# Kernel tuning notes

Measured on AMD Instinct MI355X. Metric: run time of the kernel, lower is better.

The kernel has to match this reference:

```python
import jax, jax.numpy as jnp
import numpy as np

HIDDEN = 32
N_STEPS = 64  # fixed-step RK4 replaces adaptive Dopri5 (same MLP-eval structure)
STD = 0.1     # init_params: Linear weights ~ N(0, 0.1), biases = 0


def _mlp(w1, b1, w2, b2, w3, b3, y):
    # NODE.forward: fc1 -> relu -> fc2 -> relu -> fc3 (t is unused in the source)
    h = jax.nn.relu(y @ w1 + b1)
    h = jax.nn.relu(h @ w2 + b2)
    return h @ w3 + b3


def setup_inputs() -> dict:
    key = jax.random.key(0)
    ks = jax.random.split(key, 8)
    B, D = 131072, 3
    x = jax.random.normal(ks[0], (B, D), dtype=jnp.float32)
    # eval times in (0.1, 1.0], sorted like a posterior-sample schedule
    samples = jnp.sort(
        jax.random.uniform(ks[1], (8, 1), jnp.float32, 0.1, 1.0), axis=0)
    w1 = (STD * jax.random.normal(ks[2], (D, HIDDEN))).astype(jnp.float32)
    b1 = jnp.zeros((HIDDEN,), jnp.float32)
    w2 = (STD * jax.random.normal(ks[3], (HIDDEN, HIDDEN))).astype(jnp.float32)
    b2 = jnp.zeros((HIDDEN,), jnp.float32)
    w3 = (STD * jax.random.normal(ks[4], (HIDDEN, D))).astype(jnp.float32)
    b3 = jnp.zeros((D,), jnp.float32)
    w_out = (STD * jax.random.normal(ks[5], (D, 1))).astype(jnp.float32)
    b_out = jnp.zeros((1,), jnp.float32)
    return {"x": x, "samples": samples, "w1": w1, "b1": b1, "w2": w2,
            "b2": b2, "w3": w3, "b3": b3, "w_out": w_out, "b_out": b_out}


def reference(x, samples, w1, b1, w2, b2, w3, b3, w_out, b_out):
    t_eval = samples[:, 0]                     # (S,)
    max_T = jnp.max(t_eval)
    dt = max_T / N_STEPS

    def step(y, _):
        k1 = _mlp(w1, b1, w2, b2, w3, b3, y)
        k2 = _mlp(w1, b1, w2, b2, w3, b3, y + 0.5 * dt * k1)
        k3 = _mlp(w1, b1, w2, b2, w3, b3, y + 0.5 * dt * k2)
        k4 = _mlp(w1, b1, w2, b2, w3, b3, y + dt * k3)
        y_new = y + (dt / 6.0) * (k1 + 2.0 * k2 + 2.0 * k3 + k4)
        return y_new, y_new

    # traj[i] is the state at time (i+1)*dt; shape (N_STEPS, B, 3)
    _, traj = jax.lax.scan(jax.checkpoint(step), x, jnp.arange(N_STEPS))

    # gather states at the grid step nearest each eval time
    idx = jnp.clip(jnp.round(t_eval / dt).astype(jnp.int32) - 1, 0, N_STEPS - 1)
    y_eval = traj[idx]                         # (S, B, 3)

    # fc_layers readout -> act_vec (S, B, 1)
    return y_eval @ w_out + b_out
```

## Files before the change

### kernel.cpp

```cpp
#include <hip/hip_runtime.h>

#define NSTEPS 64

typedef __attribute__((ext_vector_type(4)))  float  float4_;
typedef __attribute__((ext_vector_type(2)))  __fp16 half2_;
typedef __attribute__((ext_vector_type(8)))  __fp16 half8_;

__device__ __forceinline__ half2_ relu_pk_f16(float a, float b) {
    half2_ h = __builtin_amdgcn_cvt_pkrtz(a, b);
    return __builtin_elementwise_max(h, (half2_)(__fp16)0);
}

__global__ __launch_bounds__(64, 4)
void ode_rk4_mfma(const float* __restrict__ x,
                  const float* __restrict__ samples,
                  const float* __restrict__ w1, const float* __restrict__ b1,
                  const float* __restrict__ w2, const float* __restrict__ b2,
                  const float* __restrict__ w3, const float* __restrict__ b3,
                  const float* __restrict__ w_out, const float* __restrict__ b_out,
                  float* __restrict__ out, int B)
{
    const int lane  = threadIdx.x & 63;
    const int col16 = lane & 15;
    const int quad  = lane >> 4;

    const int row = blockIdx.x * 16 + col16;

    auto sig = [](int p) -> int {
        int q = (p & 15) >> 2, r = p & 3;
        return q * 8 + r + ((p < 16) ? 0 : 4);
    };

    const float maxT = samples[7];
    const float dt   = maxT / 64.0f;
    const float dt2  = 0.5f * dt;
    const float dt6  = dt / 6.0f;

    union F { half2_ h2[4]; half8_ h8; };

    F Mh[2], Mz[2];
#pragma unroll
    for (int H = 0; H < 2; ++H) {
        int u = sig(16 * H + col16);
#pragma unroll
        for (int pp = 0; pp < 4; ++pp) {
            int kk = quad * 8 + 2 * pp;
            float m0 = w3[kk * 3 + 0] * w1[0 * 32 + u]
                     + w3[kk * 3 + 1] * w1[1 * 32 + u]
                     + w3[kk * 3 + 2] * w1[2 * 32 + u];
            float m1 = w3[(kk + 1) * 3 + 0] * w1[0 * 32 + u]
                     + w3[(kk + 1) * 3 + 1] * w1[1 * 32 + u]
                     + w3[(kk + 1) * 3 + 2] * w1[2 * 32 + u];
            Mh[H].h2[pp] = (half2_){(__fp16)(dt2 * m0), (__fp16)(dt2 * m1)};
            Mz[H].h2[pp] = (half2_){(__fp16)(dt6 * m0), (__fp16)(dt6 * m1)};
        }
    }

    F A2[2];
    float4_ Cb[2];
#pragma unroll
    for (int H = 0; H < 2; ++H) {
        int u = sig(16 * H + col16);
#pragma unroll
        for (int pp = 0; pp < 4; ++pp) {
            int kk = quad * 8 + 2 * pp;
            A2[H].h2[pp] = (half2_){(__fp16)w2[kk * 32 + u], (__fp16)w2[(kk + 1) * 32 + u]};
        }
#pragma unroll
        for (int r = 0; r < 4; ++r)
            Cb[H][r] = b2[sig(16 * H + quad * 4 + r)];
    }

    F A3;
    {
        const int  d    = col16 & 3;
        const bool live = d < 3;
#pragma unroll
        for (int pp = 0; pp < 4; ++pp) {
            int kk = quad * 8 + 2 * pp;
            A3.h2[pp] = live
                ? (half2_){(__fp16)w3[kk * 3 + d], (__fp16)w3[(kk + 1) * 3 + d]}
                : (half2_)(__fp16)0.0f;
        }
    }
    float4_ C3;
#pragma unroll
    for (int r = 0; r < 4; ++r)
        C3[r] = (r < 3) ? 6.0f * b3[r] : 0.0f;

    float4_ cH[2];
#pragma unroll
    for (int H = 0; H < 2; ++H)
#pragma unroll
        for (int r = 0; r < 4; ++r) {
            int u = sig(16 * H + quad * 4 + r);
            cH[H][r] = dt2 * (b3[0] * w1[0 * 32 + u] + b3[1] * w1[1 * 32 + u] + b3[2] * w1[2 * 32 + u]);
        }

    int sidx[8];
    unsigned long long smask = 0ull;
#pragma unroll
    for (int j = 0; j < 8; ++j) {
        int id = (int)rintf(samples[j] / dt) - 1;
        id = id < 0 ? 0 : (id > NSTEPS - 1 ? NSTEPS - 1 : id);
        id = __builtin_amdgcn_readfirstlane(id);
        sidx[j] = id;
        smask |= 1ull << id;
    }
    const float wo0 = w_out[0], wo1 = w_out[1], wo2 = w_out[2];
    const float bo  = b_out[0];

    float y0 = x[(size_t)row * 3 + 0];
    float y1 = x[(size_t)row * 3 + 1];
    float y2 = x[(size_t)row * 3 + 2];

    float4_ zb0, zb1;
    {
        F A1y[2];
#pragma unroll
        for (int H = 0; H < 2; ++H) {
            if (quad == 0) {
                int u = sig(16 * H + col16);
                A1y[H].h2[0] = (half2_){(__fp16)w1[0 * 32 + u], (__fp16)w1[1 * 32 + u]};
                A1y[H].h2[1] = (half2_){(__fp16)w1[2 * 32 + u], (__fp16)b1[u]};
                A1y[H].h2[2] = (half2_)(__fp16)0.0f;
                A1y[H].h2[3] = (half2_)(__fp16)0.0f;
            } else {
#pragma unroll
                for (int pp = 0; pp < 4; ++pp) A1y[H].h2[pp] = (half2_)(__fp16)0.0f;
            }
        }
        float4_ Zc;
#pragma unroll
        for (int r = 0; r < 4; ++r) Zc[r] = 0.0f;
        half2_ b0a = __builtin_amdgcn_cvt_pkrtz(y0, y1);
        half2_ b0b = __builtin_amdgcn_cvt_pkrtz(y2, 1.0f);
        F By;
        By.h2[0] = b0a; By.h2[1] = b0b; By.h2[2] = b0a; By.h2[3] = b0b;
        zb0 = __builtin_amdgcn_mfma_f32_16x16x32_f16(A1y[0].h8, By.h8, Zc, 0, 0, 0);
        zb1 = __builtin_amdgcn_mfma_f32_16x16x32_f16(A1y[1].h8, By.h8, Zc, 0, 0, 0);
    }

    const half2_ two = (half2_)(__fp16)2.0f;

#pragma unroll 1
    for (int s = 0; s < NSTEPS; ++s) {
        F P, Q, S;

        P.h2[0] = relu_pk_f16(zb0[0], zb0[1]);
        P.h2[1] = relu_pk_f16(zb0[2], zb0[3]);
        P.h2[2] = relu_pk_f16(zb1[0], zb1[1]);
        P.h2[3] = relu_pk_f16(zb1[2], zb1[3]);
        __builtin_amdgcn_s_setprio(1);
        float4_ D2_0 = __builtin_amdgcn_mfma_f32_16x16x32_f16(A2[0].h8, P.h8, Cb[0], 0, 0, 0);
        float4_ D2_1 = __builtin_amdgcn_mfma_f32_16x16x32_f16(A2[1].h8, P.h8, Cb[1], 0, 0, 0);
        __builtin_amdgcn_s_setprio(0);
        Q.h2[0] = relu_pk_f16(D2_0[0], D2_0[1]);
        Q.h2[1] = relu_pk_f16(D2_0[2], D2_0[3]);
        Q.h2[2] = relu_pk_f16(D2_1[0], D2_1[1]);
        Q.h2[3] = relu_pk_f16(D2_1[2], D2_1[3]);
#pragma unroll
        for (int pp = 0; pp < 4; ++pp) S.h2[pp] = Q.h2[pp];

        float4_ zh0 = zb0 + cH[0];
        float4_ zh1 = zb1 + cH[1];

#pragma unroll
        for (int st = 1; st <= 2; ++st) {
            __builtin_amdgcn_s_setprio(1);
            float4_ D1_0 = __builtin_amdgcn_mfma_f32_16x16x32_f16(Mh[0].h8, Q.h8, zh0, 0, 0, 0);
            float4_ D1_1 = __builtin_amdgcn_mfma_f32_16x16x32_f16(Mh[1].h8, Q.h8, zh1, 0, 0, 0);
            __builtin_amdgcn_s_setprio(0);
            P.h2[0] = relu_pk_f16(D1_0[0], D1_0[1]);
            P.h2[1] = relu_pk_f16(D1_0[2], D1_0[3]);
            P.h2[2] = relu_pk_f16(D1_1[0], D1_1[1]);
            P.h2[3] = relu_pk_f16(D1_1[2], D1_1[3]);
            __builtin_amdgcn_s_setprio(1);
            float4_ E0 = __builtin_amdgcn_mfma_f32_16x16x32_f16(A2[0].h8, P.h8, Cb[0], 0, 0, 0);
            float4_ E1 = __builtin_amdgcn_mfma_f32_16x16x32_f16(A2[1].h8, P.h8, Cb[1], 0, 0, 0);
            __builtin_amdgcn_s_setprio(0);
            Q.h2[0] = relu_pk_f16(E0[0], E0[1]);
            Q.h2[1] = relu_pk_f16(E0[2], E0[3]);
            Q.h2[2] = relu_pk_f16(E1[0], E1[1]);
            Q.h2[3] = relu_pk_f16(E1[2], E1[3]);
#pragma unroll
            for (int pp = 0; pp < 4; ++pp)
                S.h2[pp] += two * Q.h2[pp];
        }

        zh0 = zh0 + cH[0];
        zh1 = zh1 + cH[1];
        F Qd;
#pragma unroll
        for (int pp = 0; pp < 4; ++pp) Qd.h2[pp] = Q.h2[pp] + Q.h2[pp];
        __builtin_amdgcn_s_setprio(1);
        float4_ D1_0 = __builtin_amdgcn_mfma_f32_16x16x32_f16(Mh[0].h8, Qd.h8, zh0, 0, 0, 0);
        float4_ D1_1 = __builtin_amdgcn_mfma_f32_16x16x32_f16(Mh[1].h8, Qd.h8, zh1, 0, 0, 0);
        __builtin_amdgcn_s_setprio(0);
        P.h2[0] = relu_pk_f16(D1_0[0], D1_0[1]);
        P.h2[1] = relu_pk_f16(D1_0[2], D1_0[3]);
        P.h2[2] = relu_pk_f16(D1_1[0], D1_1[1]);
        P.h2[3] = relu_pk_f16(D1_1[2], D1_1[3]);
        __builtin_amdgcn_s_setprio(1);
        float4_ E0 = __builtin_amdgcn_mfma_f32_16x16x32_f16(A2[0].h8, P.h8, Cb[0], 0, 0, 0);
        float4_ E1 = __builtin_amdgcn_mfma_f32_16x16x32_f16(A2[1].h8, P.h8, Cb[1], 0, 0, 0);
        __builtin_amdgcn_s_setprio(0);
        Q.h2[0] = relu_pk_f16(E0[0], E0[1]);
        Q.h2[1] = relu_pk_f16(E0[2], E0[3]);
        Q.h2[2] = relu_pk_f16(E1[0], E1[1]);
        Q.h2[3] = relu_pk_f16(E1[2], E1[3]);
#pragma unroll
        for (int pp = 0; pp < 4; ++pp) S.h2[pp] += Q.h2[pp];

        __builtin_amdgcn_s_setprio(1);
        float4_ D3 = __builtin_amdgcn_mfma_f32_16x16x32_f16(A3.h8, S.h8, C3, 0, 0, 0);
        zb0 = __builtin_amdgcn_mfma_f32_16x16x32_f16(Mz[0].h8, S.h8, zb0, 0, 0, 0);
        zb1 = __builtin_amdgcn_mfma_f32_16x16x32_f16(Mz[1].h8, S.h8, zb1, 0, 0, 0);
        __builtin_amdgcn_s_setprio(0);
#pragma unroll
        for (int r = 0; r < 4; ++r) {
            zb0[r] = fmaf(2.0f, cH[0][r], zb0[r]);
            zb1[r] = fmaf(2.0f, cH[1][r], zb1[r]);
        }
        y0 = fmaf(dt6, D3[0], y0);
        y1 = fmaf(dt6, D3[1], y1);
        y2 = fmaf(dt6, D3[2], y2);

        if ((smask >> s) & 1ull) {
            if (quad == 0) {
#pragma unroll
                for (int j = 0; j < 8; ++j) {
                    if (sidx[j] == s) {
                        out[(size_t)j * B + row] = fmaf(y2, wo2, fmaf(y1, wo1, fmaf(y0, wo0, bo)));
                    }
                }
            }
        }
    }
}

extern "C" void kernel_launch(void* const* d_in, const int* in_sizes, int n_in,
                              void* d_out, int out_size, void* d_ws, size_t ws_size,
                              hipStream_t stream) {
    const float* x       = (const float*)d_in[0];
    const float* samples = (const float*)d_in[1];
    const float* w1      = (const float*)d_in[2];
    const float* b1      = (const float*)d_in[3];
    const float* w2      = (const float*)d_in[4];
    const float* b2      = (const float*)d_in[5];
    const float* w3      = (const float*)d_in[6];
    const float* b3      = (const float*)d_in[7];
    const float* w_out   = (const float*)d_in[8];
    const float* b_out   = (const float*)d_in[9];
    float* out = (float*)d_out;

    const int B = in_sizes[0] / 3;
    const int rowsPerBlock = 16;
    const int grid = (B + rowsPerBlock - 1) / rowsPerBlock;
    ode_rk4_mfma<<<grid, 64, 0, stream>>>(
        x, samples, w1, b1, w2, b2, w3, b3, w_out, b_out, out, B);
}
```

Baseline: 208.9 us.

## Process two independent 16-row tiles per wavefront to interleave MFMA chains

Each wavefront now integrates two 16-row batches, running the RK4 step for both inside the same loop iteration. Because the two steps share no data, the compiler can interleave their dependent MFMA/ReLU chains and hide MFMA latency without relying on other waves. The s_setprio hints are removed, the grid is halved, and launch bounds drop to 3 waves per EU to make room for the doubled register state. The risk is lower occupancy and possible register pressure if the compiler serializes the two chains.

```diff
diff --git a/kernel.cpp b/kernel.cpp
--- a/kernel.cpp
+++ b/kernel.cpp
@@ -11,7 +11,7 @@
     return __builtin_elementwise_max(h, (half2_)(__fp16)0);
 }
 
-__global__ __launch_bounds__(64, 4)
+__global__ __launch_bounds__(64, 3)
 void ode_rk4_mfma(const float* __restrict__ x,
                   const float* __restrict__ samples,
                   const float* __restrict__ w1, const float* __restrict__ b1,
@@ -24,7 +24,8 @@
     const int col16 = lane & 15;
     const int quad  = lane >> 4;
 
-    const int row = blockIdx.x * 16 + col16;
+    const int rowA = blockIdx.x * 32 + col16;
+    const int rowB = rowA + 16;
 
     auto sig = [](int p) -> int {
         int q = (p & 15) >> 2, r = p & 3;
@@ -110,11 +111,14 @@
     const float wo0 = w_out[0], wo1 = w_out[1], wo2 = w_out[2];
     const float bo  = b_out[0];
 
-    float y0 = x[(size_t)row * 3 + 0];
-    float y1 = x[(size_t)row * 3 + 1];
-    float y2 = x[(size_t)row * 3 + 2];
-
-    float4_ zb0, zb1;
+    float yA0 = x[(size_t)rowA * 3 + 0];
+    float yA1 = x[(size_t)rowA * 3 + 1];
+    float yA2 = x[(size_t)rowA * 3 + 2];
+    float yB0 = x[(size_t)rowB * 3 + 0];
+    float yB1 = x[(size_t)rowB * 3 + 1];
+    float yB2 = x[(size_t)rowB * 3 + 2];
+
+    float4_ zbA0, zbA1, zbB0, zbB1;
     {
         F A1y[2];
 #pragma unroll
@@ -133,28 +137,29 @@
         float4_ Zc;
 #pragma unroll
         for (int r = 0; r < 4; ++r) Zc[r] = 0.0f;
-        half2_ b0a = __builtin_amdgcn_cvt_pkrtz(y0, y1);
-        half2_ b0b = __builtin_amdgcn_cvt_pkrtz(y2, 1.0f);
-        F By;
-        By.h2[0] = b0a; By.h2[1] = b0b; By.h2[2] = b0a; By.h2[3] = b0b;
-        zb0 = __builtin_amdgcn_mfma_f32_16x16x32_f16(A1y[0].h8, By.h8, Zc, 0, 0, 0);
-        zb1 = __builtin_amdgcn_mfma_f32_16x16x32_f16(A1y[1].h8, By.h8, Zc, 0, 0, 0);
+        half2_ aA = __builtin_amdgcn_cvt_pkrtz(yA0, yA1);
+        half2_ bA = __builtin_amdgcn_cvt_pkrtz(yA2, 1.0f);
+        half2_ aB = __builtin_amdgcn_cvt_pkrtz(yB0, yB1);
+        half2_ bB = __builtin_amdgcn_cvt_pkrtz(yB2, 1.0f);
+        F ByA, ByB;
+        ByA.h2[0] = aA; ByA.h2[1] = bA; ByA.h2[2] = aA; ByA.h2[3] = bA;
+        ByB.h2[0] = aB; ByB.h2[1] = bB; ByB.h2[2] = aB; ByB.h2[3] = bB;
+        zbA0 = __builtin_amdgcn_mfma_f32_16x16x32_f16(A1y[0].h8, ByA.h8, Zc, 0, 0, 0);
+        zbA1 = __builtin_amdgcn_mfma_f32_16x16x32_f16(A1y[1].h8, ByA.h8, Zc, 0, 0, 0);
+        zbB0 = __builtin_amdgcn_mfma_f32_16x16x32_f16(A1y[0].h8, ByB.h8, Zc, 0, 0, 0);
+        zbB1 = __builtin_amdgcn_mfma_f32_16x16x32_f16(A1y[1].h8, ByB.h8, Zc, 0, 0, 0);
     }
 
     const half2_ two = (half2_)(__fp16)2.0f;
 
-#pragma unroll 1
-    for (int s = 0; s < NSTEPS; ++s) {
+    auto rk_step = [&](float4_& zb0, float4_& zb1, float& y0, float& y1, float& y2) {
         F P, Q, S;
-
         P.h2[0] = relu_pk_f16(zb0[0], zb0[1]);
         P.h2[1] = relu_pk_f16(zb0[2], zb0[3]);
         P.h2[2] = relu_pk_f16(zb1[0], zb1[1]);
         P.h2[3] = relu_pk_f16(zb1[2], zb1[3]);
-        __builtin_amdgcn_s_setprio(1);
         float4_ D2_0 = __builtin_amdgcn_mfma_f32_16x16x32_f16(A2[0].h8, P.h8, Cb[0], 0, 0, 0);
         float4_ D2_1 = __builtin_amdgcn_mfma_f32_16x16x32_f16(A2[1].h8, P.h8, Cb[1], 0, 0, 0);
-        __builtin_amdgcn_s_setprio(0);
         Q.h2[0] = relu_pk_f16(D2_0[0], D2_0[1]);
         Q.h2[1] = relu_pk_f16(D2_0[2], D2_0[3]);
         Q.h2[2] = relu_pk_f16(D2_1[0], D2_1[1]);
@@ -167,18 +172,14 @@
 
 #pragma unroll
         for (int st = 1; st <= 2; ++st) {
-            __builtin_amdgcn_s_setprio(1);
             float4_ D1_0 = __builtin_amdgcn_mfma_f32_16x16x32_f16(Mh[0].h8, Q.h8, zh0, 0, 0, 0);
             float4_ D1_1 = __builtin_amdgcn_mfma_f32_16x16x32_f16(Mh[1].h8, Q.h8, zh1, 0, 0, 0);
-            __builtin_amdgcn_s_setprio(0);
             P.h2[0] = relu_pk_f16(D1_0[0], D1_0[1]);
             P.h2[1] = relu_pk_f16(D1_0[2], D1_0[3]);
             P.h2[2] = relu_pk_f16(D1_1[0], D1_1[1]);
             P.h2[3] = relu_pk_f16(D1_1[2], D1_1[3]);
-            __builtin_amdgcn_s_setprio(1);
             float4_ E0 = __builtin_amdgcn_mfma_f32_16x16x32_f16(A2[0].h8, P.h8, Cb[0], 0, 0, 0);
             float4_ E1 = __builtin_amdgcn_mfma_f32_16x16x32_f16(A2[1].h8, P.h8, Cb[1], 0, 0, 0);
-            __builtin_amdgcn_s_setprio(0);
             Q.h2[0] = relu_pk_f16(E0[0], E0[1]);
             Q.h2[1] = relu_pk_f16(E0[2], E0[3]);
             Q.h2[2] = relu_pk_f16(E1[0], E1[1]);
@@ -193,18 +194,14 @@
         F Qd;
 #pragma unroll
         for (int pp = 0; pp < 4; ++pp) Qd.h2[pp] = Q.h2[pp] + Q.h2[pp];
-        __builtin_amdgcn_s_setprio(1);
         float4_ D1_0 = __builtin_amdgcn_mfma_f32_16x16x32_f16(Mh[0].h8, Qd.h8, zh0, 0, 0, 0);
         float4_ D1_1 = __builtin_amdgcn_mfma_f32_16x16x32_f16(Mh[1].h8, Qd.h8, zh1, 0, 0, 0);
-        __builtin_amdgcn_s_setprio(0);
         P.h2[0] = relu_pk_f16(D1_0[0], D1_0[1]);
         P.h2[1] = relu_pk_f16(D1_0[2], D1_0[3]);
         P.h2[2] = relu_pk_f16(D1_1[0], D1_1[1]);
         P.h2[3] = relu_pk_f16(D1_1[2], D1_1[3]);
-        __builtin_amdgcn_s_setprio(1);
         float4_ E0 = __builtin_amdgcn_mfma_f32_16x16x32_f16(A2[0].h8, P.h8, Cb[0], 0, 0, 0);
         float4_ E1 = __builtin_amdgcn_mfma_f32_16x16x32_f16(A2[1].h8, P.h8, Cb[1], 0, 0, 0);
-        __builtin_amdgcn_s_setprio(0);
         Q.h2[0] = relu_pk_f16(E0[0], E0[1]);
         Q.h2[1] = relu_pk_f16(E0[2], E0[3]);
         Q.h2[2] = relu_pk_f16(E1[0], E1[1]);
@@ -212,11 +209,9 @@
 #pragma unroll
         for (int pp = 0; pp < 4; ++pp) S.h2[pp] += Q.h2[pp];
 
-        __builtin_amdgcn_s_setprio(1);
         float4_ D3 = __builtin_amdgcn_mfma_f32_16x16x32_f16(A3.h8, S.h8, C3, 0, 0, 0);
         zb0 = __builtin_amdgcn_mfma_f32_16x16x32_f16(Mz[0].h8, S.h8, zb0, 0, 0, 0);
         zb1 = __builtin_amdgcn_mfma_f32_16x16x32_f16(Mz[1].h8, S.h8, zb1, 0, 0, 0);
-        __builtin_amdgcn_s_setprio(0);
 #pragma unroll
         for (int r = 0; r < 4; ++r) {
             zb0[r] = fmaf(2.0f, cH[0][r], zb0[r]);
@@ -225,13 +220,20 @@
         y0 = fmaf(dt6, D3[0], y0);
         y1 = fmaf(dt6, D3[1], y1);
         y2 = fmaf(dt6, D3[2], y2);
+    };
+
+#pragma unroll 1
+    for (int s = 0; s < NSTEPS; ++s) {
+        rk_step(zbA0, zbA1, yA0, yA1, yA2);
+        rk_step(zbB0, zbB1, yB0, yB1, yB2);
 
         if ((smask >> s) & 1ull) {
             if (quad == 0) {
 #pragma unroll
                 for (int j = 0; j < 8; ++j) {
                     if (sidx[j] == s) {
-                        out[(size_t)j * B + row] = fmaf(y2, wo2, fmaf(y1, wo1, fmaf(y0, wo0, bo)));
+                        out[(size_t)j * B + rowA] = fmaf(yA2, wo2, fmaf(yA1, wo1, fmaf(yA0, wo0, bo)));
+                        out[(size_t)j * B + rowB] = fmaf(yB2, wo2, fmaf(yB1, wo1, fmaf(yB0, wo0, bo)));
                     }
                 }
             }
@@ -255,7 +257,7 @@
     float* out = (float*)d_out;
 
     const int B = in_sizes[0] / 3;
-    const int rowsPerBlock = 16;
+    const int rowsPerBlock = 32;
     const int grid = (B + rowsPerBlock - 1) / rowsPerBlock;
     ode_rk4_mfma<<<grid, 64, 0, stream>>>(
         x, samples, w1, b1, w2, b2, w3, b3, w_out, b_out, out, B);
```

Result: slower. 214.2 us (+2.5%).

## Accumulate stage sums in fp16 and defer the y readout to sample steps

Applied to the files above, without the earlier changes.

The per-step y update through the w3 MFMA is removed. A running fp16 sum of stage activations is kept instead, and y is rebuilt only at sample steps with one MFMA plus a linear bias term. The 2*Q doubling before the last stage is replaced by a separate Mf matrix scaled by dt, and the setprio hints are dropped. The launch changes to 4 waves per block with launch_bounds(256,5). This removes one MFMA and some scalar work from each step, but summing 64 steps in fp16 can lose precision.

```diff
diff --git a/kernel.cpp b/kernel.cpp
--- a/kernel.cpp
+++ b/kernel.cpp
@@ -11,7 +11,7 @@
     return __builtin_elementwise_max(h, (half2_)(__fp16)0);
 }
 
-__global__ __launch_bounds__(64, 4)
+__global__ __launch_bounds__(256, 5)
 void ode_rk4_mfma(const float* __restrict__ x,
                   const float* __restrict__ samples,
                   const float* __restrict__ w1, const float* __restrict__ b1,
@@ -21,10 +21,11 @@
                   float* __restrict__ out, int B)
 {
     const int lane  = threadIdx.x & 63;
+    const int w     = threadIdx.x >> 6;
     const int col16 = lane & 15;
     const int quad  = lane >> 4;
 
-    const int row = blockIdx.x * 16 + col16;
+    const int row = (blockIdx.x * 4 + w) * 16 + col16;
 
     auto sig = [](int p) -> int {
         int q = (p & 15) >> 2, r = p & 3;
@@ -38,7 +39,7 @@
 
     union F { half2_ h2[4]; half8_ h8; };
 
-    F Mh[2], Mz[2];
+    F Mh[2], Mf[2], Mz[2];
 #pragma unroll
     for (int H = 0; H < 2; ++H) {
         int u = sig(16 * H + col16);
@@ -52,6 +53,7 @@
                      + w3[(kk + 1) * 3 + 1] * w1[1 * 32 + u]
                      + w3[(kk + 1) * 3 + 2] * w1[2 * 32 + u];
             Mh[H].h2[pp] = (half2_){(__fp16)(dt2 * m0), (__fp16)(dt2 * m1)};
+            Mf[H].h2[pp] = (half2_){(__fp16)(dt  * m0), (__fp16)(dt  * m1)};
             Mz[H].h2[pp] = (half2_){(__fp16)(dt6 * m0), (__fp16)(dt6 * m1)};
         }
     }
@@ -83,10 +85,6 @@
                 : (half2_)(__fp16)0.0f;
         }
     }
-    float4_ C3;
-#pragma unroll
-    for (int r = 0; r < 4; ++r)
-        C3[r] = (r < 3) ? 6.0f * b3[r] : 0.0f;
 
     float4_ cH[2];
 #pragma unroll
@@ -109,10 +107,11 @@
     }
     const float wo0 = w_out[0], wo1 = w_out[1], wo2 = w_out[2];
     const float bo  = b_out[0];
-
-    float y0 = x[(size_t)row * 3 + 0];
-    float y1 = x[(size_t)row * 3 + 1];
-    float y2 = x[(size_t)row * 3 + 2];
+    const float db0 = dt * b3[0], db1 = dt * b3[1], db2 = dt * b3[2];
+
+    const float y00 = x[(size_t)row * 3 + 0];
+    const float y01 = x[(size_t)row * 3 + 1];
+    const float y02 = x[(size_t)row * 3 + 2];
 
     float4_ zb0, zb1;
     {
@@ -130,18 +129,19 @@
                 for (int pp = 0; pp < 4; ++pp) A1y[H].h2[pp] = (half2_)(__fp16)0.0f;
             }
         }
-        float4_ Zc;
-#pragma unroll
-        for (int r = 0; r < 4; ++r) Zc[r] = 0.0f;
-        half2_ b0a = __builtin_amdgcn_cvt_pkrtz(y0, y1);
-        half2_ b0b = __builtin_amdgcn_cvt_pkrtz(y2, 1.0f);
+        float4_ Zc = {0.f, 0.f, 0.f, 0.f};
+        half2_ a = __builtin_amdgcn_cvt_pkrtz(y00, y01);
+        half2_ b = __builtin_amdgcn_cvt_pkrtz(y02, 1.0f);
         F By;
-        By.h2[0] = b0a; By.h2[1] = b0b; By.h2[2] = b0a; By.h2[3] = b0b;
+        By.h2[0] = a; By.h2[1] = b; By.h2[2] = a; By.h2[3] = b;
         zb0 = __builtin_amdgcn_mfma_f32_16x16x32_f16(A1y[0].h8, By.h8, Zc, 0, 0, 0);
         zb1 = __builtin_amdgcn_mfma_f32_16x16x32_f16(A1y[1].h8, By.h8, Zc, 0, 0, 0);
     }
 
     const half2_ two = (half2_)(__fp16)2.0f;
+    F SSUM;
+#pragma unroll
+    for (int pp = 0; pp < 4; ++pp) SSUM.h2[pp] = (half2_)(__fp16)0.0f;
 
 #pragma unroll 1
     for (int s = 0; s < NSTEPS; ++s) {
@@ -151,87 +151,86 @@
         P.h2[1] = relu_pk_f16(zb0[2], zb0[3]);
         P.h2[2] = relu_pk_f16(zb1[0], zb1[1]);
         P.h2[3] = relu_pk_f16(zb1[2], zb1[3]);
-        __builtin_amdgcn_s_setprio(1);
-        float4_ D2_0 = __builtin_amdgcn_mfma_f32_16x16x32_f16(A2[0].h8, P.h8, Cb[0], 0, 0, 0);
-        float4_ D2_1 = __builtin_amdgcn_mfma_f32_16x16x32_f16(A2[1].h8, P.h8, Cb[1], 0, 0, 0);
-        __builtin_amdgcn_s_setprio(0);
-        Q.h2[0] = relu_pk_f16(D2_0[0], D2_0[1]);
-        Q.h2[1] = relu_pk_f16(D2_0[2], D2_0[3]);
-        Q.h2[2] = relu_pk_f16(D2_1[0], D2_1[1]);
-        Q.h2[3] = relu_pk_f16(D2_1[2], D2_1[3]);
-#pragma unroll
-        for (int pp = 0; pp < 4; ++pp) S.h2[pp] = Q.h2[pp];
+        float4_ D0 = __builtin_amdgcn_mfma_f32_16x16x32_f16(A2[0].h8, P.h8, Cb[0], 0, 0, 0);
+        float4_ D1 = __builtin_amdgcn_mfma_f32_16x16x32_f16(A2[1].h8, P.h8, Cb[1], 0, 0, 0);
+        S.h2[0] = relu_pk_f16(D0[0], D0[1]);
+        S.h2[1] = relu_pk_f16(D0[2], D0[3]);
+        S.h2[2] = relu_pk_f16(D1[0], D1[1]);
+        S.h2[3] = relu_pk_f16(D1[2], D1[3]);
 
         float4_ zh0 = zb0 + cH[0];
         float4_ zh1 = zb1 + cH[1];
 
-#pragma unroll
-        for (int st = 1; st <= 2; ++st) {
-            __builtin_amdgcn_s_setprio(1);
-            float4_ D1_0 = __builtin_amdgcn_mfma_f32_16x16x32_f16(Mh[0].h8, Q.h8, zh0, 0, 0, 0);
-            float4_ D1_1 = __builtin_amdgcn_mfma_f32_16x16x32_f16(Mh[1].h8, Q.h8, zh1, 0, 0, 0);
-            __builtin_amdgcn_s_setprio(0);
-            P.h2[0] = relu_pk_f16(D1_0[0], D1_0[1]);
-            P.h2[1] = relu_pk_f16(D1_0[2], D1_0[3]);
-            P.h2[2] = relu_pk_f16(D1_1[0], D1_1[1]);
-            P.h2[3] = relu_pk_f16(D1_1[2], D1_1[3]);
-            __builtin_amdgcn_s_setprio(1);
+        {
+            float4_ G0 = __builtin_amdgcn_mfma_f32_16x16x32_f16(Mh[0].h8, S.h8, zh0, 0, 0, 0);
+            float4_ G1 = __builtin_amdgcn_mfma_f32_16x16x32_f16(Mh[1].h8, S.h8, zh1, 0, 0, 0);
+            P.h2[0] = relu_pk_f16(G0[0], G0[1]);
+            P.h2[1] = relu_pk_f16(G0[2], G0[3]);
+            P.h2[2] = relu_pk_f16(G1[0], G1[1]);
+            P.h2[3] = relu_pk_f16(G1[2], G1[3]);
             float4_ E0 = __builtin_amdgcn_mfma_f32_16x16x32_f16(A2[0].h8, P.h8, Cb[0], 0, 0, 0);
             float4_ E1 = __builtin_amdgcn_mfma_f32_16x16x32_f16(A2[1].h8, P.h8, Cb[1], 0, 0, 0);
-            __builtin_amdgcn_s_setprio(0);
             Q.h2[0] = relu_pk_f16(E0[0], E0[1]);
             Q.h2[1] = relu_pk_f16(E0[2], E0[3]);
             Q.h2[2] = relu_pk_f16(E1[0], E1[1]);
             Q.h2[3] = relu_pk_f16(E1[2], E1[3]);
 #pragma unroll
-            for (int pp = 0; pp < 4; ++pp)
-                S.h2[pp] += two * Q.h2[pp];
+            for (int pp = 0; pp < 4; ++pp) S.h2[pp] += two * Q.h2[pp];
+        }
+
+        {
+            float4_ G0 = __builtin_amdgcn_mfma_f32_16x16x32_f16(Mh[0].h8, Q.h8, zh0, 0, 0, 0);
+            float4_ G1 = __builtin_amdgcn_mfma_f32_16x16x32_f16(Mh[1].h8, Q.h8, zh1, 0, 0, 0);
+            P.h2[0] = relu_pk_f16(G0[0], G0[1]);
+            P.h2[1] = relu_pk_f16(G0[2], G0[3]);
+            P.h2[2] = relu_pk_f16(G1[0], G1[1]);
+            P.h2[3] = relu_pk_f16(G1[2], G1[3]);
+            float4_ E0 = __builtin_amdgcn_mfma_f32_16x16x32_f16(A2[0].h8, P.h8, Cb[0], 0, 0, 0);
+            float4_ E1 = __builtin_amdgcn_mfma_f32_16x16x32_f16(A2[1].h8, P.h8, Cb[1], 0, 0, 0);
+            Q.h2[0] = relu_pk_f16(E0[0], E0[1]);
+            Q.h2[1] = relu_pk_f16(E0[2], E0[3]);
+            Q.h2[2] = relu_pk_f16(E1[0], E1[1]);
+            Q.h2[3] = relu_pk_f16(E1[2], E1[3]);
+#pragma unroll
+            for (int pp = 0; pp < 4; ++pp) S.h2[pp] += two * Q.h2[pp];
         }
 
         zh0 = zh0 + cH[0];
         zh1 = zh1 + cH[1];
-        F Qd;
-#pragma unroll
-        for (int pp = 0; pp < 4; ++pp) Qd.h2[pp] = Q.h2[pp] + Q.h2[pp];
-        __builtin_amdgcn_s_setprio(1);
-        float4_ D1_0 = __builtin_amdgcn_mfma_f32_16x16x32_f16(Mh[0].h8, Qd.h8, zh0, 0, 0, 0);
-        float4_ D1_1 = __builtin_amdgcn_mfma_f32_16x16x32_f16(Mh[1].h8, Qd.h8, zh1, 0, 0, 0);
-        __builtin_amdgcn_s_setprio(0);
-        P.h2[0] = relu_pk_f16(D1_0[0], D1_0[1]);
-        P.h2[1] = relu_pk_f16(D1_0[2], D1_0[3]);
-        P.h2[2] = relu_pk_f16(D1_1[0], D1_1[1]);
-        P.h2[3] = relu_pk_f16(D1_1[2], D1_1[3]);
-        __builtin_amdgcn_s_setprio(1);
-        float4_ E0 = __builtin_amdgcn_mfma_f32_16x16x32_f16(A2[0].h8, P.h8, Cb[0], 0, 0, 0);
-        float4_ E1 = __builtin_amdgcn_mfma_f32_16x16x32_f16(A2[1].h8, P.h8, Cb[1], 0, 0, 0);
-        __builtin_amdgcn_s_setprio(0);
-        Q.h2[0] = relu_pk_f16(E0[0], E0[1]);
-        Q.h2[1] = relu_pk_f16(E0[2], E0[3]);
-        Q.h2[2] = relu_pk_f16(E1[0], E1[1]);
-        Q.h2[3] = relu_pk_f16(E1[2], E1[3]);
-#pragma unroll
-        for (int pp = 0; pp < 4; ++pp) S.h2[pp] += Q.h2[pp];
-
-        __builtin_amdgcn_s_setprio(1);
-        float4_ D3 = __builtin_amdgcn_mfma_f32_16x16x32_f16(A3.h8, S.h8, C3, 0, 0, 0);
-        zb0 = __builtin_amdgcn_mfma_f32_16x16x32_f16(Mz[0].h8, S.h8, zb0, 0, 0, 0);
-        zb1 = __builtin_amdgcn_mfma_f32_16x16x32_f16(Mz[1].h8, S.h8, zb1, 0, 0, 0);
-        __builtin_amdgcn_s_setprio(0);
-#pragma unroll
-        for (int r = 0; r < 4; ++r) {
-            zb0[r] = fmaf(2.0f, cH[0][r], zb0[r]);
-            zb1[r] = fmaf(2.0f, cH[1][r], zb1[r]);
-        }
-        y0 = fmaf(dt6, D3[0], y0);
-        y1 = fmaf(dt6, D3[1], y1);
-        y2 = fmaf(dt6, D3[2], y2);
+        {
+            float4_ G0 = __builtin_amdgcn_mfma_f32_16x16x32_f16(Mf[0].h8, Q.h8, zh0, 0, 0, 0);
+            float4_ G1 = __builtin_amdgcn_mfma_f32_16x16x32_f16(Mf[1].h8, Q.h8, zh1, 0, 0, 0);
+            P.h2[0] = relu_pk_f16(G0[0], G0[1]);
+            P.h2[1] = relu_pk_f16(G0[2], G0[3]);
+            P.h2[2] = relu_pk_f16(G1[0], G1[1]);
+            P.h2[3] = relu_pk_f16(G1[2], G1[3]);
+            float4_ E0 = __builtin_amdgcn_mfma_f32_16x16x32_f16(A2[0].h8, P.h8, Cb[0], 0, 0, 0);
+            float4_ E1 = __builtin_amdgcn_mfma_f32_16x16x32_f16(A2[1].h8, P.h8, Cb[1], 0, 0, 0);
+            Q.h2[0] = relu_pk_f16(E0[0], E0[1]);
+            Q.h2[1] = relu_pk_f16(E0[2], E0[3]);
+            Q.h2[2] = relu_pk_f16(E1[0], E1[1]);
+            Q.h2[3] = relu_pk_f16(E1[2], E1[3]);
+#pragma unroll
+            for (int pp = 0; pp < 4; ++pp) S.h2[pp] += Q.h2[pp];
+        }
+
+#pragma unroll
+        for (int pp = 0; pp < 4; ++pp) SSUM.h2[pp] += S.h2[pp];
+        zb0 = __builtin_amdgcn_mfma_f32_16x16x32_f16(Mz[0].h8, S.h8, zh0, 0, 0, 0);
+        zb1 = __builtin_amdgcn_mfma_f32_16x16x32_f16(Mz[1].h8, S.h8, zh1, 0, 0, 0);
 
         if ((smask >> s) & 1ull) {
+            float4_ Zc = {0.f, 0.f, 0.f, 0.f};
+            float4_ D3 = __builtin_amdgcn_mfma_f32_16x16x32_f16(A3.h8, SSUM.h8, Zc, 0, 0, 0);
+            float T = (float)(s + 1);
+            float o0 = fmaf(dt6, D3[0], fmaf(T, db0, y00));
+            float o1 = fmaf(dt6, D3[1], fmaf(T, db1, y01));
+            float o2 = fmaf(dt6, D3[2], fmaf(T, db2, y02));
             if (quad == 0) {
 #pragma unroll
                 for (int j = 0; j < 8; ++j) {
                     if (sidx[j] == s) {
-                        out[(size_t)j * B + row] = fmaf(y2, wo2, fmaf(y1, wo1, fmaf(y0, wo0, bo)));
+                        out[(size_t)j * B + row] = fmaf(o2, wo2, fmaf(o1, wo1, fmaf(o0, wo0, bo)));
                     }
                 }
             }
@@ -255,8 +254,8 @@
     float* out = (float*)d_out;
 
     const int B = in_sizes[0] / 3;
-    const int rowsPerBlock = 16;
+    const int rowsPerBlock = 64;
     const int grid = (B + rowsPerBlock - 1) / rowsPerBlock;
-    ode_rk4_mfma<<<grid, 64, 0, stream>>>(
+    ode_rk4_mfma<<<grid, 256, 0, stream>>>(
         x, samples, w1, b1, w2, b2, w3, b3, w_out, b_out, out, B);
 }
```

After: 205.5 us. No clear change (-1.6%).
